# Kernel optimization log

Hardware: AMD Instinct MI355X
Metric: run time of the kernel (lower is better)

The kernel has to match this reference:

```python
import math
import jax, jax.numpy as jnp
import numpy as np

EMBED_DIM = 1024
NUM_HEADS = 16
SEGMENT_LENGTHS = [1024, 1024, 2048, 4096]
DILATION_RATES = [1, 2, 4, 8]
BATCH = 2
SEQ_LEN = 8192


def _xy2d(n, x, y):
    # Vectorized Hilbert curve xy -> d for an n x n grid (n power of 2).
    x = x.astype(np.int64).copy()
    y = y.astype(np.int64).copy()
    d = np.zeros_like(x)
    s = n // 2
    while s > 0:
        rx = ((x & s) > 0).astype(np.int64)
        ry = ((y & s) > 0).astype(np.int64)
        d += s * s * ((3 * rx) ^ ry)
        swap = ry == 0
        flip = swap & (rx == 1)
        x = np.where(flip, s - 1 - x, x)
        y = np.where(flip, s - 1 - y, y)
        xs = np.where(swap, y, x)
        ys = np.where(swap, x, y)
        x, y = xs, ys
        s //= 2
    return d


def _hilbert_perm(L):
    # Returns (perm, inv): new[i] = old[perm[i]] (Hilbert order), inv undoes it.
    if L <= 1:
        p = np.arange(L, dtype=np.int64)
        return p, p
    side = 1 << int(math.ceil(math.log2(L) / 2.0))  # side^2 >= L
    idx = np.arange(side * side, dtype=np.int64)
    xg = idx % side
    yg = idx // side
    d = _xy2d(side, xg, yg)
    order = np.argsort(d, kind='stable')  # linear cell indices in Hilbert order
    perm = order[order < L]
    inv = np.empty(L, dtype=np.int64)
    inv[perm] = np.arange(L, dtype=np.int64)
    return perm, inv


def _dilated_attention(q, k, v, rate, scale):
    # q,k,v: [B,H,L,D]; attention within residue-class groups (positions i with i % rate == j).
    B, H, L, D = q.shape
    if rate > 1:
        g = L // rate
        q = q.reshape(B, H, g, rate, D).transpose(0, 1, 3, 2, 4)  # [B,H,r,g,D]
        k = k.reshape(B, H, g, rate, D).transpose(0, 1, 3, 2, 4)
        v = v.reshape(B, H, g, rate, D).transpose(0, 1, 3, 2, 4)
    scores = jnp.einsum('...qd,...kd->...qk', q, k) * scale
    attn = jax.nn.softmax(scores, axis=-1)
    out = jnp.einsum('...qk,...kd->...qd', attn, v)
    if rate > 1:
        out = out.transpose(0, 1, 3, 2, 4).reshape(B, H, L, D)
    return out


def _forward(x, w_qkv, b_qkv, w_out, b_out):
    B, S, E = x.shape
    H = NUM_HEADS
    Dh = E // H
    scale = 1.0 / math.sqrt(Dh)
    qkv = x @ w_qkv.T + b_qkv                       # [B,S,3E]
    qkv = qkv.reshape(B, S, 3, H, Dh).transpose(2, 0, 3, 1, 4)  # [3,B,H,S,Dh]
    q, k, v = qkv[0], qkv[1], qkv[2]
    outs = []
    pos = 0
    for seg_len, rate in zip(SEGMENT_LENGTHS, DILATION_RATES):
        if pos >= S:
            break
        end = min(pos + seg_len, S)
        L = end - pos
        qs = q[:, :, pos:end]
        ks = k[:, :, pos:end]
        vs = v[:, :, pos:end]
        if L > 1:
            perm_np, inv_np = _hilbert_perm(L)
            perm = jnp.asarray(perm_np)
            inv = jnp.asarray(inv_np)
            qs = qs[:, :, perm]
            ks = ks[:, :, perm]
            vs = vs[:, :, perm]
        seg_out = _dilated_attention(qs, ks, vs, rate, scale)
        if L > 1:
            seg_out = seg_out[:, :, inv]
        outs.append(seg_out)
        pos = end
    out = jnp.concatenate(outs, axis=2)             # [B,H,S,Dh]
    out = out.transpose(0, 2, 1, 3).reshape(B, S, E)
    return out @ w_out.T + b_out


def setup_inputs() -> dict:
    key = jax.random.key(0)
    k1, k2, k3 = jax.random.split(key, 3)
    E = EMBED_DIM
    return {
        'x': jax.random.normal(k1, (BATCH, SEQ_LEN, E), dtype=jnp.float32),
        'w_qkv': jax.random.normal(k2, (3 * E, E), dtype=jnp.float32) * 0.02,
        'b_qkv': jnp.zeros((3 * E,), dtype=jnp.float32),
        'w_out': jax.random.normal(k3, (E, E), dtype=jnp.float32) * 0.02,
        'b_out': jnp.zeros((E,), dtype=jnp.float32),
    }


def reference(x, w_qkv, b_qkv, w_out, b_out):
    return _forward(x, w_qkv, b_qkv, w_out, b_out)
```

## Files before the change

### kernel.cpp

```cpp
#include <hip/hip_runtime.h>
#include <hip/hip_bf16.h>
#include <math.h>

#define S_LEN 8192
#define NH 16
#define DH 64
#define BB 2
#define EE 1024

typedef float floatx4 __attribute__((ext_vector_type(4)));
typedef float f32x4 __attribute__((ext_vector_type(4)));
typedef short bf16x8 __attribute__((ext_vector_type(8)));
typedef _Float16 f16x8 __attribute__((ext_vector_type(8)));
typedef int i32x4 __attribute__((ext_vector_type(4)));
typedef unsigned short u16x4 __attribute__((ext_vector_type(4)));

__device__ inline unsigned short f2bf(float x) {
  unsigned int u = __builtin_bit_cast(unsigned int, x);
  u += 0x7FFFu + ((u >> 16) & 1u);
  return (unsigned short)(u >> 16);
}
__device__ inline float bf2f(unsigned short h) {
  return __builtin_bit_cast(float, (unsigned int)h << 16);
}

__device__ inline void async_copy16(void* lds, const void* g) {
  __builtin_amdgcn_global_load_lds(
      (const __attribute__((address_space(1))) void*)g,
      (__attribute__((address_space(3))) void*)lds, 16, 0, 0);
}

__device__ inline int hilbert_xy2d(int n, int x, int y) {
  int d = 0;
  for (int s = n >> 1; s > 0; s >>= 1) {
    int rx = (x & s) ? 1 : 0;
    int ry = (y & s) ? 1 : 0;
    d += s * s * ((3 * rx) ^ ry);
    if (ry == 0) {
      if (rx == 1) { x = s - 1 - x; y = s - 1 - y; }
      int t = x; x = y; y = t;
    }
  }
  return d;
}

__global__ void build_idx_kernel(int* __restrict__ idx) {
  __shared__ int order[4096];
  __shared__ int perm[4096];
  __shared__ int cnts[256];
  const int seg = blockIdx.x;
  const int posA[4] = {0, 1024, 2048, 4096};
  const int LA[4]   = {1024, 1024, 2048, 4096};
  const int pos = posA[seg];
  const int L = LA[seg];
  const int lr = seg;
  const int side  = (L <= 1024) ? 32 : 64;
  const int lside = (L <= 1024) ? 5 : 6;
  const int cells = side * side;
  const int tid = threadIdx.x;

  for (int c = tid; c < cells; c += 256) {
    int x = c & (side - 1);
    int y = c >> lside;
    order[hilbert_xy2d(side, x, y)] = c;
  }
  __syncthreads();

  if (L == cells) {
    for (int t = tid; t < L; t += 256) perm[t] = order[t];
  } else {
    const int per = cells >> 8;
    const int base = tid * per;
    int cnt = 0;
    for (int u = 0; u < per; ++u) cnt += (order[base + u] < L) ? 1 : 0;
    cnts[tid] = cnt;
    __syncthreads();
    if (tid == 0) {
      int s = 0;
      for (int i = 0; i < 256; ++i) { int c0 = cnts[i]; cnts[i] = s; s += c0; }
    }
    __syncthreads();
    int r = cnts[tid];
    for (int u = 0; u < per; ++u) {
      int o = order[base + u];
      if (o < L) perm[r++] = o;
    }
  }
  __syncthreads();

  const int g = L >> lr;
  const int rm = (1 << lr) - 1;
  for (int t = tid; t < L; t += 256) {
    int j = t & rm;
    int i = t >> lr;
    idx[pos + j * g + i] = pos + perm[t];
  }
}

__global__ __launch_bounds__(256) void tof16_kernel(
    const float* __restrict__ in, unsigned short* __restrict__ hi, int n) {
  int base = (blockIdx.x * 256 + threadIdx.x) * 8;
  if (base >= n) return;
  floatx4 v0 = *(const floatx4*)(in + base);
  floatx4 v1 = *(const floatx4*)(in + base + 4);
  u16x4 h0, h1;
#pragma unroll
  for (int i = 0; i < 4; ++i) {
    h0[i] = __builtin_bit_cast(unsigned short, (_Float16)v0[i]);
    h1[i] = __builtin_bit_cast(unsigned short, (_Float16)v1[i]);
  }
  *(u16x4*)(hi + base) = h0;
  *(u16x4*)(hi + base + 4) = h1;
}

template<int MODE>
__global__ __launch_bounds__(256, 2) void mgemm_kernel(
    const unsigned short* __restrict__ Ah, const unsigned short* __restrict__ Bh,
    const float* __restrict__ bias, float* __restrict__ Cf,
    unsigned short* __restrict__ q_h, unsigned short* __restrict__ k_h,
    unsigned short* __restrict__ v_h,
    int N, int K) {
  __shared__ short lds[2][12288];
  const int tid = threadIdx.x;
  const int lane = tid & 63;
  const int w = tid >> 6;
  const int wr = w >> 1, wc = w & 1;
  const int bm0 = blockIdx.x * 128;
  const int bn0 = blockIdx.y * 256;

  const unsigned short* sp[6];
  int dofs[6];
#pragma unroll
  for (int ii = 0; ii < 6; ++ii) {
    int e = w * 6 + ii;
    const unsigned short* base = (e < 8) ? Ah : Bh;
    int row0 = (e < 8) ? (bm0 + e * 16) : (bn0 + (e - 8) * 16);
    int dof = (e < 8) ? (e * 512) : (4096 + (e - 8) * 512);
    sp[ii] = base + (size_t)(row0 + (lane & 15)) * K + (lane >> 4) * 8;
    dofs[ii] = dof;
  }

  f32x4 acc[4][8];
#pragma unroll
  for (int m = 0; m < 4; ++m)
#pragma unroll
    for (int n = 0; n < 8; ++n) acc[m][n] = (f32x4)0.f;

  const int nk = K >> 5;
#pragma unroll
  for (int ii = 0; ii < 6; ++ii) async_copy16(&lds[0][dofs[ii]], sp[ii]);
#pragma unroll
  for (int ii = 0; ii < 6; ++ii) async_copy16(&lds[1][dofs[ii]], sp[ii] + 32);
  asm volatile("s_waitcnt vmcnt(6)" ::: "memory");
  __builtin_amdgcn_s_barrier();

  for (int t = 0; t < nk; ++t) {
    const short* lb = &lds[t & 1][0];

    f16x8 ah[4], bf[8];
#pragma unroll
    for (int m = 0; m < 4; ++m)
      ah[m] = *(const f16x8*)&lb[(wr * 4 + m) * 512 + lane * 8];
#pragma unroll
    for (int n = 0; n < 8; ++n)
      bf[n] = *(const f16x8*)&lb[4096 + (wc * 8 + n) * 512 + lane * 8];

    asm volatile("s_waitcnt lgkmcnt(0)" ::: "memory");
    __builtin_amdgcn_s_barrier();

    if (t + 2 < nk) {
      short* db = &lds[t & 1][0];
      const int k0 = (t + 2) * 32;
#pragma unroll
      for (int ii = 0; ii < 6; ++ii) async_copy16(db + dofs[ii], sp[ii] + k0);
    }

    __builtin_amdgcn_s_setprio(1);
#pragma unroll
    for (int m = 0; m < 4; ++m)
#pragma unroll
      for (int n = 0; n < 8; ++n)
        acc[m][n] = __builtin_amdgcn_mfma_f32_16x16x32_f16(ah[m], bf[n], acc[m][n], 0, 0, 0);
    __builtin_amdgcn_s_setprio(0);

    if (t + 2 < nk) {
      asm volatile("s_waitcnt vmcnt(6)" ::: "memory");
    } else {
      asm volatile("s_waitcnt vmcnt(0)" ::: "memory");
    }
    if (t + 1 < nk) __builtin_amdgcn_s_barrier();
  }

  const int rq = lane >> 4;
  const int cl = lane & 15;
#pragma unroll
  for (int n = 0; n < 8; ++n) {
    const int gn = bn0 + wc * 128 + n * 16 + cl;
    const float bv = bias[gn];
    if (MODE == 0) {
      const int which = gn >> 10;
      const int hh = (gn >> 6) & 15;
      const int d = gn & 63;
      const float scale = (which == 0) ? 0.125f : 1.0f;
      unsigned short* dsth = (which == 0) ? q_h : (which == 1) ? k_h : v_h;
#pragma unroll
      for (int m = 0; m < 4; ++m)
#pragma unroll
        for (int j = 0; j < 4; ++j) {
          const int gm = bm0 + wr * 64 + m * 16 + rq * 4 + j;
          const int b = gm >> 13;
          const int s = gm & 8191;
          float val = (acc[m][n][j] + bv) * scale;
          size_t off = ((size_t)(b * NH + hh) * S_LEN + s) * DH + d;
          dsth[off] = f2bf(val);
        }
    } else {
#pragma unroll
      for (int m = 0; m < 4; ++m)
#pragma unroll
        for (int j = 0; j < 4; ++j) {
          const int gm = bm0 + wr * 64 + m * 16 + rq * 4 + j;
          Cf[(size_t)gm * N + gn] = acc[m][n][j] + bv;
        }
    }
  }
}

__global__ __launch_bounds__(256, 2) void mattn_kernel(
    const unsigned short* __restrict__ qh, const unsigned short* __restrict__ kh,
    const unsigned short* __restrict__ vh, const int* __restrict__ idx,
    unsigned short* __restrict__ oh) {
  __shared__ __align__(16) char smem[53248];
  int* idxg = (int*)(smem + 49152);

  const int tid = threadIdx.x;
  const int lane = tid & 63;
  const int w = tid >> 6;
  const int g = lane >> 4;
  const int q = lane & 15;

  const int c = blockIdx.x;
  const int bh = blockIdx.y;
  const int bb = bh >> 4;
  const int h = bh & 15;
  int gbase, glen, q0;
  if (c < 4) { gbase = 0; glen = 1024; q0 = c * 256; }
  else { int t = c - 4; gbase = 1024 + (t >> 1) * 512; glen = 512; q0 = (t & 1) * 256; }

  for (int i = tid; i < glen; i += 256) idxg[i] = idx[gbase + i];
  __syncthreads();

  const size_t bhoff = (size_t)(bb * NH + h) * S_LEN * DH;
  const unsigned short* qhb = qh + bhoff;
  const unsigned short* khb = kh + bhoff;
  const unsigned short* vhb = vh + bhoff;

  int qrow[4];
#pragma unroll
  for (int qt = 0; qt < 4; ++qt) qrow[qt] = idxg[q0 + w * 64 + qt * 16 + q];

  f32x4 oacc[4][4];
#pragma unroll
  for (int dt = 0; dt < 4; ++dt)
#pragma unroll
    for (int qt = 0; qt < 4; ++qt) oacc[dt][qt] = (f32x4)0.f;
  float mq[4] = {-1e30f, -1e30f, -1e30f, -1e30f};
  float lq[4] = {0.f, 0.f, 0.f, 0.f};

  const int rem = tid & 127;
  const int p = rem & 31;
  const int dh = (rem >> 5) * 16;
  char* vb = smem + 32768;

  bf16x8 VA0, VA1, VB0, VB1;

#pragma unroll
  for (int ii = 0; ii < 2; ++ii) {
    int g8 = w * 2 + ii;
    int r = g8 * 8 + (lane >> 3);
    int bsw = (lane & 7) ^ (r & 7);
    async_copy16(smem + g8 * 1024, khb + (size_t)idxg[r] * DH + bsw * 8);
  }
  if (tid < 128) {
    int r0 = idxg[2 * p], r1 = idxg[2 * p + 1];
    VA0 = *(const bf16x8*)(vhb + (size_t)r0 * DH + dh);
    VA1 = *(const bf16x8*)(vhb + (size_t)r0 * DH + dh + 8);
    VB0 = *(const bf16x8*)(vhb + (size_t)r1 * DH + dh);
    VB1 = *(const bf16x8*)(vhb + (size_t)r1 * DH + dh + 8);
  }

  const int nt = glen >> 6;
  for (int kt_ = 0; kt_ < nt; ++kt_) {
    const int kt0 = kt_ * 64;
    const char* kb = smem + (kt_ & 1) * 16384;

    asm volatile("s_waitcnt vmcnt(0)" ::: "memory");
    __builtin_amdgcn_s_barrier();

    if (tid < 128) {
#pragma unroll
      for (int u = 0; u < 16; ++u) {
        unsigned short a = (unsigned short)((u < 8) ? VA0[u] : VA1[u - 8]);
        unsigned short b2 = (unsigned short)((u < 8) ? VB0[u] : VB1[u - 8]);
        unsigned int w32 = (unsigned int)a | ((unsigned int)b2 << 16);
        int d = dh + u;
        int byte_ = (d * 128 + p * 4) ^ ((d & 7) << 4);
        *(unsigned int*)(vb + byte_) = w32;
      }
    }

    if (kt_ + 1 < nt) {
      char* kbn = smem + ((kt_ + 1) & 1) * 16384;
#pragma unroll
      for (int ii = 0; ii < 2; ++ii) {
        int g8 = w * 2 + ii;
        int r = g8 * 8 + (lane >> 3);
        int bsw = (lane & 7) ^ (r & 7);
        async_copy16(kbn + g8 * 1024,
                     khb + (size_t)idxg[kt0 + 64 + r] * DH + bsw * 8);
      }
      if (tid < 128) {
        int r0 = idxg[kt0 + 64 + 2 * p], r1 = idxg[kt0 + 64 + 2 * p + 1];
        VA0 = *(const bf16x8*)(vhb + (size_t)r0 * DH + dh);
        VA1 = *(const bf16x8*)(vhb + (size_t)r0 * DH + dh + 8);
        VB0 = *(const bf16x8*)(vhb + (size_t)r1 * DH + dh);
        VB1 = *(const bf16x8*)(vhb + (size_t)r1 * DH + dh + 8);
      }
    }

    asm volatile("s_waitcnt lgkmcnt(0)" ::: "memory");
    __builtin_amdgcn_s_barrier();

    f32x4 sacc[4][4];
#pragma unroll
    for (int qt = 0; qt < 4; ++qt)
#pragma unroll
      for (int kt = 0; kt < 4; ++kt) sacc[qt][kt] = (f32x4)0.f;
#pragma unroll
    for (int dc = 0; dc < 2; ++dc) {
      bf16x8 kf[4];
#pragma unroll
      for (int kt = 0; kt < 4; ++kt) {
        int r = q + 16 * kt;
        int byte_ = (r * 128 + g * 16 + dc * 64) ^ ((r & 7) << 4);
        kf[kt] = *(const bf16x8*)(kb + byte_);
      }
#pragma unroll
      for (int qt = 0; qt < 4; ++qt) {
        bf16x8 qhf = *(const bf16x8*)(qhb + (size_t)qrow[qt] * DH + dc * 32 + g * 8);
#pragma unroll
        for (int kt = 0; kt < 4; ++kt)
          sacc[qt][kt] = __builtin_amdgcn_mfma_f32_16x16x32_bf16(kf[kt], qhf, sacc[qt][kt], 0, 0, 0);
      }
    }

    i32x4 pfh[4][2];
#pragma unroll
    for (int qt = 0; qt < 4; ++qt) {
      float mold = mq[qt];
      float tm = -1e30f;
#pragma unroll
      for (int kt = 0; kt < 4; ++kt)
#pragma unroll
        for (int j = 0; j < 4; ++j) tm = fmaxf(tm, sacc[qt][kt][j]);
      tm = fmaxf(tm, __shfl_xor(tm, 16));
      tm = fmaxf(tm, __shfl_xor(tm, 32));
      float mn = fmaxf(mold, tm);
      float su = 0.f;
#pragma unroll
      for (int kt = 0; kt < 4; ++kt)
#pragma unroll
        for (int j = 0; j < 4; ++j) {
          float pv = __expf(sacc[qt][kt][j] - mn);
          sacc[qt][kt][j] = pv;
          su += pv;
        }
      su += __shfl_xor(su, 16);
      su += __shfl_xor(su, 32);
      float rs = __expf(mold - mn);
      lq[qt] = lq[qt] * rs + su;
      mq[qt] = mn;
      if (__any(mn > mold)) {
#pragma unroll
        for (int dt = 0; dt < 4; ++dt) oacc[dt][qt] *= rs;
      }
      unsigned int eh[4][2];
#pragma unroll
      for (int kt = 0; kt < 4; ++kt)
#pragma unroll
        for (int pp = 0; pp < 2; ++pp) {
          unsigned int ba = (unsigned int)f2bf(sacc[qt][kt][2 * pp]);
          unsigned int bb2 = (unsigned int)f2bf(sacc[qt][kt][2 * pp + 1]);
          eh[kt][pp] = ba | (bb2 << 16);
        }
#pragma unroll
      for (int kc = 0; kc < 2; ++kc) {
        i32x4 fh;
#pragma unroll
        for (int t = 0; t < 4; ++t) {
          int src = q + 32 * (g & 1) + 16 * (t >> 1);
          int ah = __shfl((int)eh[2 * kc][t & 1], src);
          int bh2 = __shfl((int)eh[2 * kc + 1][t & 1], src);
          fh[t] = (g >> 1) ? bh2 : ah;
        }
        pfh[qt][kc] = fh;
      }
    }

#pragma unroll
    for (int kc = 0; kc < 2; ++kc)
#pragma unroll
      for (int dt = 0; dt < 4; ++dt) {
        int r = q + 16 * dt;
        int byte_ = (r * 128 + g * 16 + kc * 64) ^ ((r & 7) << 4);
        bf16x8 vf = *(const bf16x8*)(vb + byte_);
#pragma unroll
        for (int qt = 0; qt < 4; ++qt) {
          bf16x8 ph = __builtin_bit_cast(bf16x8, pfh[qt][kc]);
          oacc[dt][qt] = __builtin_amdgcn_mfma_f32_16x16x32_bf16(vf, ph, oacc[dt][qt], 0, 0, 0);
        }
      }
  }

#pragma unroll
  for (int qt = 0; qt < 4; ++qt) {
    float inv = 1.f / lq[qt];
    size_t obase = ((size_t)bb * S_LEN + qrow[qt]) * EE + h * DH;
#pragma unroll
    for (int dt = 0; dt < 4; ++dt) {
      u16x4 hv;
#pragma unroll
      for (int j = 0; j < 4; ++j)
        hv[j] = __builtin_bit_cast(unsigned short, (_Float16)(oacc[dt][qt][j] * inv));
      *(u16x4*)(oh + obase + dt * 16 + g * 4) = hv;
    }
  }
}

extern "C" void kernel_launch(void* const* d_in, const int* in_sizes, int n_in,
                              void* d_out, int out_size, void* d_ws, size_t ws_size,
                              hipStream_t stream) {
  const float* x     = (const float*)d_in[0];
  const float* w_qkv = (const float*)d_in[1];
  const float* b_qkv = (const float*)d_in[2];
  const float* w_out = (const float*)d_in[3];
  const float* b_out = (const float*)d_in[4];
  float* outp = (float*)d_out;

  const size_t per = (size_t)BB * S_LEN * EE;
  const size_t nwq = (size_t)3 * EE * EE;
  const size_t nwo = (size_t)EE * EE;

  unsigned short* khb = (unsigned short*)d_ws;
  unsigned short* vhb = khb + per;
  unsigned short* xh  = vhb + per;
  unsigned short* wqh = xh + per;
  unsigned short* woh = wqh + nwq;
  int* idx = (int*)(woh + nwo);

  unsigned short* qhb = (unsigned short*)d_out;
  unsigned short* ah  = xh;

  build_idx_kernel<<<4, 256, 0, stream>>>(idx);
  tof16_kernel<<<(int)(per / 2048), 256, 0, stream>>>(x, xh, (int)per);
  tof16_kernel<<<(int)(nwq / 2048), 256, 0, stream>>>(w_qkv, wqh, (int)nwq);
  tof16_kernel<<<(int)(nwo / 2048), 256, 0, stream>>>(w_out, woh, (int)nwo);

  mgemm_kernel<0><<<dim3(128, 12), 256, 0, stream>>>(
      xh, wqh, b_qkv, nullptr, qhb, khb, vhb, 3 * EE, EE);
  mattn_kernel<<<dim3(32, 32), 256, 0, stream>>>(qhb, khb, vhb, idx, ah);
  mgemm_kernel<1><<<dim3(128, 4), 256, 0, stream>>>(
      ah, woh, b_out, outp, nullptr, nullptr, nullptr, EE, EE);
}
```

Baseline: 416.5 us.

## Use exp2 with folded log2e scale, lazy max rescale, and fp16 PV path

Folds log2(e) into the Q scale so the softmax can use the native exp2 instruction instead of __expf. Adds a lazy-rescale threshold: the running max and the output rescale are skipped unless a new score exceeds the old max by more than 8 (in log2 units). V and P are now stored as fp16, and the PV product uses the f16 MFMA, which avoids the manual bf16 rounding of probabilities. The attention kernel's launch bounds go from 2 to 3 blocks per SM, which may cause register spills. fp16 V adds some overflow risk, and the unnormalised probabilities can grow up to 2^8.

```diff
diff --git a/kernel.cpp b/kernel.cpp
--- a/kernel.cpp
+++ b/kernel.cpp
@@ -19,9 +19,6 @@
   unsigned int u = __builtin_bit_cast(unsigned int, x);
   u += 0x7FFFu + ((u >> 16) & 1u);
   return (unsigned short)(u >> 16);
-}
-__device__ inline float bf2f(unsigned short h) {
-  return __builtin_bit_cast(float, (unsigned int)h << 16);
 }
 
 __device__ inline void async_copy16(void* lds, const void* g) {
@@ -201,7 +198,6 @@
       const int which = gn >> 10;
       const int hh = (gn >> 6) & 15;
       const int d = gn & 63;
-      const float scale = (which == 0) ? 0.125f : 1.0f;
       unsigned short* dsth = (which == 0) ? q_h : (which == 1) ? k_h : v_h;
 #pragma unroll
       for (int m = 0; m < 4; ++m)
@@ -210,9 +206,14 @@
           const int gm = bm0 + wr * 64 + m * 16 + rq * 4 + j;
           const int b = gm >> 13;
           const int s = gm & 8191;
-          float val = (acc[m][n][j] + bv) * scale;
+          float val = acc[m][n][j] + bv;
           size_t off = ((size_t)(b * NH + hh) * S_LEN + s) * DH + d;
-          dsth[off] = f2bf(val);
+          if (which == 2) {
+            dsth[off] = __builtin_bit_cast(unsigned short, (_Float16)val);
+          } else {
+            float sc = (which == 0) ? 0.18033688f : 1.0f;
+            dsth[off] = f2bf(val * sc);
+          }
         }
     } else {
 #pragma unroll
@@ -226,7 +227,7 @@
   }
 }
 
-__global__ __launch_bounds__(256, 2) void mattn_kernel(
+__global__ __launch_bounds__(256, 3) void mattn_kernel(
     const unsigned short* __restrict__ qh, const unsigned short* __restrict__ kh,
     const unsigned short* __restrict__ vh, const int* __restrict__ idx,
     unsigned short* __restrict__ oh) {
@@ -365,32 +366,37 @@
         for (int j = 0; j < 4; ++j) tm = fmaxf(tm, sacc[qt][kt][j]);
       tm = fmaxf(tm, __shfl_xor(tm, 16));
       tm = fmaxf(tm, __shfl_xor(tm, 32));
-      float mn = fmaxf(mold, tm);
+      bool nores = __all(tm <= mold + 8.f);
+      float mn = nores ? mold : fmaxf(mold, tm);
       float su = 0.f;
 #pragma unroll
       for (int kt = 0; kt < 4; ++kt)
 #pragma unroll
         for (int j = 0; j < 4; ++j) {
-          float pv = __expf(sacc[qt][kt][j] - mn);
+          float pv = __builtin_amdgcn_exp2f(sacc[qt][kt][j] - mn);
           sacc[qt][kt][j] = pv;
           su += pv;
         }
       su += __shfl_xor(su, 16);
       su += __shfl_xor(su, 32);
-      float rs = __expf(mold - mn);
-      lq[qt] = lq[qt] * rs + su;
-      mq[qt] = mn;
-      if (__any(mn > mold)) {
+      if (nores) {
+        lq[qt] += su;
+      } else {
+        float rs = __builtin_amdgcn_exp2f(mold - mn);
+        lq[qt] = lq[qt] * rs + su;
 #pragma unroll
         for (int dt = 0; dt < 4; ++dt) oacc[dt][qt] *= rs;
+        mq[qt] = mn;
       }
       unsigned int eh[4][2];
 #pragma unroll
       for (int kt = 0; kt < 4; ++kt)
 #pragma unroll
         for (int pp = 0; pp < 2; ++pp) {
-          unsigned int ba = (unsigned int)f2bf(sacc[qt][kt][2 * pp]);
-          unsigned int bb2 = (unsigned int)f2bf(sacc[qt][kt][2 * pp + 1]);
+          unsigned int ba =
+              (unsigned int)__builtin_bit_cast(unsigned short, (_Float16)sacc[qt][kt][2 * pp]);
+          unsigned int bb2 =
+              (unsigned int)__builtin_bit_cast(unsigned short, (_Float16)sacc[qt][kt][2 * pp + 1]);
           eh[kt][pp] = ba | (bb2 << 16);
         }
 #pragma unroll
@@ -413,11 +419,11 @@
       for (int dt = 0; dt < 4; ++dt) {
         int r = q + 16 * dt;
         int byte_ = (r * 128 + g * 16 + kc * 64) ^ ((r & 7) << 4);
-        bf16x8 vf = *(const bf16x8*)(vb + byte_);
+        f16x8 vf = *(const f16x8*)(vb + byte_);
 #pragma unroll
         for (int qt = 0; qt < 4; ++qt) {
-          bf16x8 ph = __builtin_bit_cast(bf16x8, pfh[qt][kc]);
-          oacc[dt][qt] = __builtin_amdgcn_mfma_f32_16x16x32_bf16(vf, ph, oacc[dt][qt], 0, 0, 0);
+          f16x8 ph = __builtin_bit_cast(f16x8, pfh[qt][kc]);
+          oacc[dt][qt] = __builtin_amdgcn_mfma_f32_16x16x32_f16(vf, ph, oacc[dt][qt], 0, 0, 0);
         }
       }
   }
```

After: 596.2 us. +43.1%, slower.
